# Performance work log

Hardware: AMD Instinct MI355X
Metric: run time of the kernel (lower is better)

Reference implementation:

```python
import jax, jax.numpy as jnp
import numpy as np

N = 4096
E = 131072
IN_CH, E_CH, HID, OUT = 512, 64, 256, 16
K, J = 2, 3
REWEIGHT = ((E_CH + HID) / (IN_CH + HID)) ** 0.5


def gcn(x, W, b, src, dst, dinv):
    # x: [B, N, F] -> [B, N, H]; symmetric-normalized aggregation with self-loops (PyG GCNConv)
    h = x @ W
    norm = dinv[src] * dinv[dst]                      # [E]
    msg = jnp.take(h, src, axis=-2) * norm[:, None]   # [B, E, H]
    agg = jnp.zeros_like(h).at[:, dst, :].add(msg)
    out = agg + h * (dinv * dinv)[:, None]            # self-loop term, norm_ii = deg_i^-1
    return out + b


def setup_inputs() -> dict:
    key = jax.random.key(0)
    ks = jax.random.split(key, 12)
    x = jax.random.normal(ks[0], (1, N, IN_CH), jnp.float32)
    edge_index = jax.random.randint(ks[1], (2, E), 0, N)
    e_noise = jax.random.normal(ks[2], (K + J, N, E_CH), jnp.float32)
    eps = jax.random.normal(ks[3], (J, N, OUT), jnp.float32)
    def glorot(k, fan_in, fan_out):
        s = (6.0 / (fan_in + fan_out)) ** 0.5
        return jax.random.uniform(k, (fan_in, fan_out), jnp.float32, -s, s)
    W1 = glorot(ks[4], IN_CH, HID); b1 = jnp.zeros((HID,), jnp.float32)
    We = glorot(ks[5], E_CH, HID); be = jnp.zeros((HID,), jnp.float32)
    Wmu = glorot(ks[6], HID, OUT); bmu = jnp.zeros((OUT,), jnp.float32)
    Wsig = glorot(ks[7], HID, OUT); bsig = jnp.zeros((OUT,), jnp.float32)
    rk_lgt = jax.random.uniform(ks[8], (1, OUT), jnp.float32, -6.0, 0.0)
    return {"x": x, "edge_index": edge_index, "e_noise": e_noise, "eps": eps,
            "W1": W1, "b1": b1, "We": We, "be": be,
            "Wmu": Wmu, "bmu": bmu, "Wsig": Wsig, "bsig": bsig, "rk_lgt": rk_lgt}


def reference(x, edge_index, e_noise, eps, W1, b1, We, be, Wmu, bmu, Wsig, bsig, rk_lgt):
    src, dst = edge_index[0], edge_index[1]
    deg = jnp.zeros((N,), jnp.float32).at[dst].add(1.0) + 1.0  # self-loops
    dinv = jax.lax.rsqrt(deg)

    hidden_x = jax.nn.relu(gcn(x, W1, b1, src, dst, dinv))          # [1, N, HID]
    e = e_noise * REWEIGHT                                          # [K+J, N, E_CH]
    hidden_e = gcn(e, We, be, src, dst, dinv)                       # [K+J, N, HID]
    hidden1 = hidden_x + hidden_e                                   # [K+J, N, HID]

    p_signal = jnp.mean(hidden_x ** 2)
    p_noise = jnp.mean(hidden_e ** 2, axis=(-2, -1))                # [K+J]
    snr = p_signal / p_noise

    mu = gcn(hidden1, Wmu, bmu, src, dst, dinv)                     # [K+J, N, OUT]
    sigma = gcn(hidden1, Wsig, bsig, src, dst, dinv)                # [K+J, N, OUT]

    emb_mu = mu[K:]
    emb_logvar = sigma[K:]
    std = jnp.exp(emb_logvar * 0.5)
    z = eps * std + emb_mu                                          # [J, N, OUT]

    # GraphDecoder, gdc='ip', dropout=0 (eval): z_scaled = z, adj = sigmoid(z z^T)
    rk = jnp.sqrt(jax.nn.sigmoid(rk_lgt))                           # [1, OUT]
    adj_lgt = jnp.einsum('bnd,bmd->bnm', z, z)                      # [J, N, N]
    adj_ = jax.nn.sigmoid(adj_lgt)
    z_scaled = z
    return (adj_, mu, sigma, z, z_scaled, eps, rk, snr)
```

## Files before the change

### kernel.cpp

```cpp
#include <hip/hip_runtime.h>

#define NN     4096
#define NE     131072
#define IN_CH  512
#define E_CH   64
#define HID    256
#define OUT_CH 16
#define KK     2
#define JJ     3
#define NB     5
#define REWEIGHT 0.6454972243679028f

#define O_ADJ  0L
#define O_MU   50331648L
#define O_SG   50659328L
#define O_Z    50987008L
#define O_ZS   51183616L
#define O_EPS  51380224L
#define O_RK   51576832L
#define O_SNR  51576848L


__global__ void k_deg(const int* __restrict__ dst, int* __restrict__ degi) {
    int i = blockIdx.x * 256 + threadIdx.x;
    if (i < NE) atomicAdd(&degi[dst[i]], 1);
}

__global__ void k_scan(const int* __restrict__ degi, int* __restrict__ rowptr,
                       int* __restrict__ cursor) {
    __shared__ int sums[1024];
    int t = threadIdx.x;
    int v[4];
    int s = 0;
#pragma unroll
    for (int i = 0; i < 4; ++i) { v[i] = s; s += degi[t * 4 + i]; }
    sums[t] = s;
    __syncthreads();
    for (int off = 1; off < 1024; off <<= 1) {
        int a = (t >= off) ? sums[t - off] : 0;
        __syncthreads();
        sums[t] += a;
        __syncthreads();
    }
    int base = (t > 0) ? sums[t - 1] : 0;
#pragma unroll
    for (int i = 0; i < 4; ++i) {
        rowptr[t * 4 + i] = base + v[i];
        cursor[t * 4 + i] = base + v[i];
    }
    if (t == 1023) rowptr[4096] = sums[1023];
}

__global__ void k_dinv(const int* __restrict__ degi, float* __restrict__ dinv) {
    int i = blockIdx.x * 256 + threadIdx.x;
    if (i < NN) dinv[i] = rsqrtf((float)degi[i] + 1.0f);
}

__global__ void k_fill(const int* __restrict__ src, const int* __restrict__ dst,
                       const float* __restrict__ dinv,
                       int* __restrict__ cursor, int* __restrict__ esrc,
                       float* __restrict__ enorm) {
    int i = blockIdx.x * 256 + threadIdx.x;
    if (i >= NE) return;
    int s = src[i], d = dst[i];
    int pos = atomicAdd(&cursor[d], 1);
    esrc[pos] = s;
    enorm[pos] = dinv[s] * dinv[d];
}


__global__ void k_gemm_x(const float* __restrict__ x, const float* __restrict__ W1,
                         float* __restrict__ h) {
    __shared__ float xs[4][IN_CH];
    long r0 = (long)blockIdx.x * 4;
    int c = threadIdx.x;
    for (int idx = c; idx < 4 * IN_CH; idx += 256) {
        int rr = idx >> 9, k = idx & 511;
        xs[rr][k] = x[(r0 + rr) * IN_CH + k];
    }
    __syncthreads();
    float acc[4] = {};
#pragma unroll 4
    for (int k = 0; k < IN_CH; ++k) {
        float w = W1[k * HID + c];
#pragma unroll
        for (int rr = 0; rr < 4; ++rr) acc[rr] = fmaf(xs[rr][k], w, acc[rr]);
    }
#pragma unroll
    for (int rr = 0; rr < 4; ++rr) h[(r0 + rr) * HID + c] = acc[rr];
}

__global__ void __launch_bounds__(64) k_agg_e(const float* __restrict__ e,
                        const int* __restrict__ rowptr, const int* __restrict__ esrc,
                        const float* __restrict__ enorm, const float* __restrict__ dinv,
                        float* __restrict__ u) {
    int n = blockIdx.x, b = blockIdx.y;
    int c = threadIdx.x;
    int beg = rowptr[n], end = rowptr[n + 1];
    float dv = dinv[n];
    const float* eb = &e[(long)b * NN * E_CH];
    float acc = eb[(long)n * E_CH + c] * dv * dv;
    for (int j = beg; j < end; ++j)
        acc = fmaf(eb[(long)esrc[j] * E_CH + c], enorm[j], acc);
    u[((long)b * NN + n) * E_CH + c] = acc * REWEIGHT;
}

__global__ void k_gemm_e(const float* __restrict__ u, const float* __restrict__ We,
                         const float* __restrict__ be, float* __restrict__ he,
                         float* __restrict__ psum) {
    __shared__ float us[8][E_CH];
    long r0 = (long)blockIdx.x * 8;
    int c = threadIdx.x;
    for (int idx = c; idx < 8 * E_CH; idx += 256) {
        int rr = idx >> 6, k = idx & 63;
        us[rr][k] = u[(r0 + rr) * E_CH + k];
    }
    __syncthreads();
    float acc[8] = {};
#pragma unroll
    for (int k = 0; k < E_CH; ++k) {
        float w = We[k * HID + c];
#pragma unroll
        for (int rr = 0; rr < 8; ++rr) acc[rr] = fmaf(us[rr][k], w, acc[rr]);
    }
    float bias = be[c];
    float sq = 0.f;
#pragma unroll
    for (int rr = 0; rr < 8; ++rr) {
        float v = acc[rr] + bias;
        he[(r0 + rr) * HID + c] = v;
        sq += v * v;
    }
#pragma unroll
    for (int off = 32; off; off >>= 1) sq += __shfl_down(sq, off, 64);
    __shared__ float red[4];
    if ((threadIdx.x & 63) == 0) red[threadIdx.x >> 6] = sq;
    __syncthreads();
    if (threadIdx.x == 0) {
        int b = blockIdx.x >> 9;
        atomicAdd(&psum[1 + b], red[0] + red[1] + red[2] + red[3]);
    }
}

__global__ void k_agg_x(const float* __restrict__ h, const int* __restrict__ rowptr,
                        const int* __restrict__ esrc, const float* __restrict__ enorm,
                        const float* __restrict__ dinv, const float* __restrict__ b1,
                        float* __restrict__ hx, float* __restrict__ psum) {
    int n = blockIdx.x;
    int c = threadIdx.x;
    int beg = rowptr[n], end = rowptr[n + 1];
    float dv = dinv[n];
    float acc = h[(long)n * HID + c] * dv * dv + b1[c];
    for (int j = beg; j < end; ++j)
        acc = fmaf(h[(long)esrc[j] * HID + c], enorm[j], acc);
    acc = fmaxf(acc, 0.f);
    hx[(long)n * HID + c] = acc;
    float sq = acc * acc;
#pragma unroll
    for (int off = 32; off; off >>= 1) sq += __shfl_down(sq, off, 64);
    __shared__ float red[4];
    if ((threadIdx.x & 63) == 0) red[threadIdx.x >> 6] = sq;
    __syncthreads();
    if (threadIdx.x == 0) atomicAdd(&psum[0], red[0] + red[1] + red[2] + red[3]);
}

__global__ void k_gemm_ms(const float* __restrict__ hx, const float* __restrict__ he,
                          const float* __restrict__ Wmu, const float* __restrict__ Wsg,
                          float* __restrict__ hmu, float* __restrict__ hsg) {
    int o = threadIdx.x & 15;
    int nn = threadIdx.x >> 4;
    int n = blockIdx.x * 16 + nn;
    int b = blockIdx.y;
    const float* px = &hx[(long)n * HID];
    const float* pe = &he[((long)b * NN + n) * HID];
    float amu = 0.f, asg = 0.f;
#pragma unroll 4
    for (int k = 0; k < HID; ++k) {
        float h1 = px[k] + pe[k];
        amu = fmaf(h1, Wmu[k * OUT_CH + o], amu);
        asg = fmaf(h1, Wsg[k * OUT_CH + o], asg);
    }
    long idx = ((long)b * NN + n) * OUT_CH + o;
    hmu[idx] = amu;
    hsg[idx] = asg;
}

__global__ void k_agg16(const int* __restrict__ rowptr, const int* __restrict__ esrc,
                        const float* __restrict__ enorm, const float* __restrict__ dinv,
                        const float* __restrict__ hmu, const float* __restrict__ hsg,
                        const float* __restrict__ bmu, const float* __restrict__ bsg,
                        float* __restrict__ omu, float* __restrict__ osg) {
    int n = blockIdx.x, b = blockIdx.y;
    int t = threadIdx.x;
    int es = t >> 4, c = t & 15;
    int beg = rowptr[n], end = rowptr[n + 1];
    const float* pm = &hmu[(long)b * NN * OUT_CH];
    const float* ps = &hsg[(long)b * NN * OUT_CH];
    float am = 0.f, as = 0.f;
    for (int j = beg + es; j < end; j += 16) {
        int s = esrc[j];
        float w = enorm[j];
        am = fmaf(pm[(long)s * OUT_CH + c], w, am);
        as = fmaf(ps[(long)s * OUT_CH + c], w, as);
    }
    am += __shfl_xor(am, 16, 64); as += __shfl_xor(as, 16, 64);
    am += __shfl_xor(am, 32, 64); as += __shfl_xor(as, 32, 64);
    __shared__ float rm[4][16], rs[4][16];
    int w = t >> 6;
    if ((t & 63) < 16) { rm[w][t & 15] = am; rs[w][t & 15] = as; }
    __syncthreads();
    float dv = dinv[n];
    float d2 = dv * dv;
    long base = ((long)b * NN + n) * OUT_CH;
    if (t < 16) {
        float v = rm[0][t] + rm[1][t] + rm[2][t] + rm[3][t]
                + pm[(long)n * OUT_CH + t] * d2 + bmu[t];
        omu[base + t] = v;
    } else if (t < 32) {
        int c2 = t - 16;
        float v = rs[0][c2] + rs[1][c2] + rs[2][c2] + rs[3][c2]
                + ps[(long)n * OUT_CH + c2] * d2 + bsg[c2];
        osg[base + c2] = v;
    }
}


__global__ void k_z(const float* __restrict__ omu, const float* __restrict__ osg,
                    const float* __restrict__ eps,
                    float* __restrict__ oz, float* __restrict__ ozs, float* __restrict__ oeps) {
    long i = (long)blockIdx.x * 256 + threadIdx.x;
    float mu = omu[(long)KK * NN * OUT_CH + i];
    float lv = osg[(long)KK * NN * OUT_CH + i];
    float ep = eps[i];
    float z = fmaf(ep, expf(0.5f * lv), mu);
    oz[i] = z;
    ozs[i] = z;
    oeps[i] = ep;
}

__global__ void k_tail(const float* __restrict__ rk_lgt, const float* __restrict__ psum,
                       float* __restrict__ ork, float* __restrict__ osnr) {
    int t = threadIdx.x;
    if (t < 16) ork[t] = sqrtf(1.f / (1.f + expf(-rk_lgt[t])));
    if (t >= 16 && t < 16 + NB) osnr[t - 16] = psum[0] / psum[1 + (t - 16)];
}

__global__ void k_adj(const float* __restrict__ z, float* __restrict__ adj) {
    __shared__ float za[64][17];
    __shared__ float zb[64][17];
    int b  = blockIdx.z;
    int bi = blockIdx.y;
    int bj = blockIdx.x;
    const float* zbase = &z[(long)b * NN * OUT_CH];
    int tid = threadIdx.x;
    for (int l = tid; l < 64 * 16; l += 256) {
        int r = l >> 4, c = l & 15;
        za[r][c] = zbase[((long)bi * 64 + r) * OUT_CH + c];
        zb[r][c] = zbase[((long)bj * 64 + r) * OUT_CH + c];
    }
    __syncthreads();
    int tr = tid >> 4, tc = tid & 15;
    float acc[4][4] = {};
#pragma unroll
    for (int d = 0; d < OUT_CH; ++d) {
        float av[4], bv[4];
#pragma unroll
        for (int i = 0; i < 4; ++i) av[i] = za[tr * 4 + i][d];
#pragma unroll
        for (int j = 0; j < 4; ++j) bv[j] = zb[tc * 4 + j][d];
#pragma unroll
        for (int i = 0; i < 4; ++i)
#pragma unroll
            for (int j = 0; j < 4; ++j) acc[i][j] = fmaf(av[i], bv[j], acc[i][j]);
    }
#pragma unroll
    for (int i = 0; i < 4; ++i) {
        long row = (long)bi * 64 + tr * 4 + i;
        float4 o;
        o.x = 1.f / (1.f + expf(-acc[i][0]));
        o.y = 1.f / (1.f + expf(-acc[i][1]));
        o.z = 1.f / (1.f + expf(-acc[i][2]));
        o.w = 1.f / (1.f + expf(-acc[i][3]));
        *reinterpret_cast<float4*>(&adj[((long)b * NN + row) * NN + (long)bj * 64 + tc * 4]) = o;
    }
}


extern "C" void kernel_launch(void* const* d_in, const int* in_sizes, int n_in,
                              void* d_out, int out_size, void* d_ws, size_t ws_size,
                              hipStream_t stream) {
    const float* x      = (const float*)d_in[0];
    const int*   eidx   = (const int*)d_in[1];
    const float* enoise = (const float*)d_in[2];
    const float* eps    = (const float*)d_in[3];
    const float* W1     = (const float*)d_in[4];
    const float* b1     = (const float*)d_in[5];
    const float* We     = (const float*)d_in[6];
    const float* be     = (const float*)d_in[7];
    const float* Wmu    = (const float*)d_in[8];
    const float* bmu    = (const float*)d_in[9];
    const float* Wsg    = (const float*)d_in[10];
    const float* bsg    = (const float*)d_in[11];
    const float* rk_lgt = (const float*)d_in[12];

    const int* src = eidx;
    const int* dst = eidx + NE;

    float* out = (float*)d_out;
    char*  ws  = (char*)d_ws;

    int*   degi   = (int*)ws;
    int*   rowptr = degi + 4096;
    int*   cursor = rowptr + 4097 + 3;
    int*   esrc   = cursor + 4096;
    float* enorm  = (float*)(esrc + NE);
    float* dinv   = enorm + NE;
    float* psum   = dinv + 4096;
    float* h_x    = psum + 16;
    float* hx     = h_x + (long)NN * HID;
    float* u_e    = hx + (long)NN * HID;
    float* he     = u_e + (long)NB * NN * E_CH;
    float* h_mu   = he + (long)NB * NN * HID;
    float* h_sg   = h_mu + (long)NB * NN * OUT_CH;

    float* omu = out + O_MU;
    float* osg = out + O_SG;

    hipMemsetAsync(degi, 0, NN * sizeof(int), stream);
    hipMemsetAsync(psum, 0, 16 * sizeof(float), stream);

    k_deg<<<NE / 256, 256, 0, stream>>>(dst, degi);
    k_scan<<<1, 1024, 0, stream>>>(degi, rowptr, cursor);
    k_dinv<<<NN / 256, 256, 0, stream>>>(degi, dinv);
    k_fill<<<NE / 256, 256, 0, stream>>>(src, dst, dinv, cursor, esrc, enorm);

    k_gemm_x<<<NN / 4, 256, 0, stream>>>(x, W1, h_x);
    k_agg_x<<<NN, 256, 0, stream>>>(h_x, rowptr, esrc, enorm, dinv, b1, hx, psum);

    k_agg_e<<<dim3(NN, NB), 64, 0, stream>>>(enoise, rowptr, esrc, enorm, dinv, u_e);
    k_gemm_e<<<NB * NN / 8, 256, 0, stream>>>(u_e, We, be, he, psum);

    k_gemm_ms<<<dim3(NN / 16, NB), 256, 0, stream>>>(hx, he, Wmu, Wsg, h_mu, h_sg);
    k_agg16<<<dim3(NN, NB), 256, 0, stream>>>(rowptr, esrc, enorm, dinv,
                                              h_mu, h_sg, bmu, bsg, omu, osg);

    k_z<<<(long)JJ * NN * OUT_CH / 256, 256, 0, stream>>>(omu, osg, eps,
                                                          out + O_Z, out + O_ZS, out + O_EPS);
    k_tail<<<1, 64, 0, stream>>>(rk_lgt, psum, out + O_RK, out + O_SNR);

    k_adj<<<dim3(NN / 64, NN / 64, JJ), 256, 0, stream>>>(out + O_Z, out);
}
```

Baseline: 549.9 us.

## Fuse small kernels, batch edge aggregation, enlarge adjacency tiles with fast sigmoid

Folds dinv computation into the scan kernel and the rk/snr tail into k_z, removing two launches. k_agg_e now handles all five noise batches per node so the edge indices and weights are read once. k_agg16 gives each node a single wavefront, which drops the shared-memory reduction and the barrier. k_adj moves to 128x128 tiles with transposed shared memory and 8x8 register blocking, and replaces expf plus division with __expf and a hardware reciprocal. k_gemm_x processes 8 rows per block. The fast sigmoid is slightly less accurate, and the larger register tiles raise register pressure.

```diff
diff --git a/kernel.cpp b/kernel.cpp
--- a/kernel.cpp
+++ b/kernel.cpp
@@ -20,20 +20,26 @@
 #define O_RK   51576832L
 #define O_SNR  51576848L
 
+__device__ __forceinline__ float fast_sigmoid(float x) {
+    float e = __expf(-x);
+    return __builtin_amdgcn_rcpf(1.f + e);
+}
+
 
 __global__ void k_deg(const int* __restrict__ dst, int* __restrict__ degi) {
     int i = blockIdx.x * 256 + threadIdx.x;
     if (i < NE) atomicAdd(&degi[dst[i]], 1);
 }
 
-__global__ void k_scan(const int* __restrict__ degi, int* __restrict__ rowptr,
-                       int* __restrict__ cursor) {
+__global__ void __launch_bounds__(1024) k_scan(const int* __restrict__ degi,
+                       int* __restrict__ rowptr, int* __restrict__ cursor,
+                       float* __restrict__ dinv) {
     __shared__ int sums[1024];
     int t = threadIdx.x;
-    int v[4];
+    int d0[4], v[4];
     int s = 0;
 #pragma unroll
-    for (int i = 0; i < 4; ++i) { v[i] = s; s += degi[t * 4 + i]; }
+    for (int i = 0; i < 4; ++i) { d0[i] = degi[t * 4 + i]; v[i] = s; s += d0[i]; }
     sums[t] = s;
     __syncthreads();
     for (int off = 1; off < 1024; off <<= 1) {
@@ -47,13 +53,9 @@
     for (int i = 0; i < 4; ++i) {
         rowptr[t * 4 + i] = base + v[i];
         cursor[t * 4 + i] = base + v[i];
+        dinv[t * 4 + i] = rsqrtf((float)d0[i] + 1.0f);
     }
     if (t == 1023) rowptr[4096] = sums[1023];
-}
-
-__global__ void k_dinv(const int* __restrict__ degi, float* __restrict__ dinv) {
-    int i = blockIdx.x * 256 + threadIdx.x;
-    if (i < NN) dinv[i] = rsqrtf((float)degi[i] + 1.0f);
 }
 
 __global__ void k_fill(const int* __restrict__ src, const int* __restrict__ dst,
@@ -69,80 +71,29 @@
 }
 
 
-__global__ void k_gemm_x(const float* __restrict__ x, const float* __restrict__ W1,
-                         float* __restrict__ h) {
-    __shared__ float xs[4][IN_CH];
-    long r0 = (long)blockIdx.x * 4;
+__global__ void __launch_bounds__(256) k_gemm_x(const float* __restrict__ x,
+                         const float* __restrict__ W1, float* __restrict__ h) {
+    __shared__ float xs[8][IN_CH];
+    long r0 = (long)blockIdx.x * 8;
     int c = threadIdx.x;
-    for (int idx = c; idx < 4 * IN_CH; idx += 256) {
+    for (int idx = c; idx < 8 * IN_CH; idx += 256) {
         int rr = idx >> 9, k = idx & 511;
         xs[rr][k] = x[(r0 + rr) * IN_CH + k];
     }
     __syncthreads();
-    float acc[4] = {};
+    float acc[8] = {};
 #pragma unroll 4
     for (int k = 0; k < IN_CH; ++k) {
         float w = W1[k * HID + c];
 #pragma unroll
-        for (int rr = 0; rr < 4; ++rr) acc[rr] = fmaf(xs[rr][k], w, acc[rr]);
-    }
-#pragma unroll
-    for (int rr = 0; rr < 4; ++rr) h[(r0 + rr) * HID + c] = acc[rr];
-}
-
-__global__ void __launch_bounds__(64) k_agg_e(const float* __restrict__ e,
-                        const int* __restrict__ rowptr, const int* __restrict__ esrc,
-                        const float* __restrict__ enorm, const float* __restrict__ dinv,
-                        float* __restrict__ u) {
-    int n = blockIdx.x, b = blockIdx.y;
-    int c = threadIdx.x;
-    int beg = rowptr[n], end = rowptr[n + 1];
-    float dv = dinv[n];
-    const float* eb = &e[(long)b * NN * E_CH];
-    float acc = eb[(long)n * E_CH + c] * dv * dv;
-    for (int j = beg; j < end; ++j)
-        acc = fmaf(eb[(long)esrc[j] * E_CH + c], enorm[j], acc);
-    u[((long)b * NN + n) * E_CH + c] = acc * REWEIGHT;
-}
-
-__global__ void k_gemm_e(const float* __restrict__ u, const float* __restrict__ We,
-                         const float* __restrict__ be, float* __restrict__ he,
-                         float* __restrict__ psum) {
-    __shared__ float us[8][E_CH];
-    long r0 = (long)blockIdx.x * 8;
-    int c = threadIdx.x;
-    for (int idx = c; idx < 8 * E_CH; idx += 256) {
-        int rr = idx >> 6, k = idx & 63;
-        us[rr][k] = u[(r0 + rr) * E_CH + k];
-    }
-    __syncthreads();
-    float acc[8] = {};
-#pragma unroll
-    for (int k = 0; k < E_CH; ++k) {
-        float w = We[k * HID + c];
-#pragma unroll
-        for (int rr = 0; rr < 8; ++rr) acc[rr] = fmaf(us[rr][k], w, acc[rr]);
-    }
-    float bias = be[c];
-    float sq = 0.f;
-#pragma unroll
-    for (int rr = 0; rr < 8; ++rr) {
-        float v = acc[rr] + bias;
-        he[(r0 + rr) * HID + c] = v;
-        sq += v * v;
-    }
-#pragma unroll
-    for (int off = 32; off; off >>= 1) sq += __shfl_down(sq, off, 64);
-    __shared__ float red[4];
-    if ((threadIdx.x & 63) == 0) red[threadIdx.x >> 6] = sq;
-    __syncthreads();
-    if (threadIdx.x == 0) {
-        int b = blockIdx.x >> 9;
-        atomicAdd(&psum[1 + b], red[0] + red[1] + red[2] + red[3]);
-    }
-}
-
-__global__ void k_agg_x(const float* __restrict__ h, const int* __restrict__ rowptr,
+        for (int rr = 0; rr < 8; ++rr) acc[rr] = fmaf(xs[rr][k], w, acc[rr]);
+    }
+#pragma unroll
+    for (int rr = 0; rr < 8; ++rr) h[(r0 + rr) * HID + c] = acc[rr];
+}
+
+__global__ void __launch_bounds__(256) k_agg_x(const float* __restrict__ h,
+                        const int* __restrict__ rowptr,
                         const int* __restrict__ esrc, const float* __restrict__ enorm,
                         const float* __restrict__ dinv, const float* __restrict__ b1,
                         float* __restrict__ hx, float* __restrict__ psum) {
@@ -164,7 +115,70 @@
     if (threadIdx.x == 0) atomicAdd(&psum[0], red[0] + red[1] + red[2] + red[3]);
 }
 
-__global__ void k_gemm_ms(const float* __restrict__ hx, const float* __restrict__ he,
+__global__ void __launch_bounds__(256) k_agg_e(const float* __restrict__ e,
+                        const int* __restrict__ rowptr, const int* __restrict__ esrc,
+                        const float* __restrict__ enorm, const float* __restrict__ dinv,
+                        float* __restrict__ u) {
+    int n = blockIdx.x * 4 + (threadIdx.x >> 6);
+    int c = threadIdx.x & 63;
+    int beg = rowptr[n], end = rowptr[n + 1];
+    float dv = dinv[n];
+    float d2 = dv * dv;
+    float acc[NB];
+#pragma unroll
+    for (int b = 0; b < NB; ++b) acc[b] = e[((long)b * NN + n) * E_CH + c] * d2;
+    for (int j = beg; j < end; ++j) {
+        int s = esrc[j];
+        float w = enorm[j];
+        long base = (long)s * E_CH + c;
+#pragma unroll
+        for (int b = 0; b < NB; ++b)
+            acc[b] = fmaf(e[(long)b * NN * E_CH + base], w, acc[b]);
+    }
+#pragma unroll
+    for (int b = 0; b < NB; ++b) u[((long)b * NN + n) * E_CH + c] = acc[b] * REWEIGHT;
+}
+
+__global__ void __launch_bounds__(256) k_gemm_e(const float* __restrict__ u,
+                         const float* __restrict__ We,
+                         const float* __restrict__ be, float* __restrict__ he,
+                         float* __restrict__ psum) {
+    __shared__ float us[8][E_CH];
+    long r0 = (long)blockIdx.x * 8;
+    int c = threadIdx.x;
+    for (int idx = c; idx < 8 * E_CH; idx += 256) {
+        int rr = idx >> 6, k = idx & 63;
+        us[rr][k] = u[(r0 + rr) * E_CH + k];
+    }
+    __syncthreads();
+    float acc[8] = {};
+#pragma unroll
+    for (int k = 0; k < E_CH; ++k) {
+        float w = We[k * HID + c];
+#pragma unroll
+        for (int rr = 0; rr < 8; ++rr) acc[rr] = fmaf(us[rr][k], w, acc[rr]);
+    }
+    float bias = be[c];
+    float sq = 0.f;
+#pragma unroll
+    for (int rr = 0; rr < 8; ++rr) {
+        float v = acc[rr] + bias;
+        he[(r0 + rr) * HID + c] = v;
+        sq += v * v;
+    }
+#pragma unroll
+    for (int off = 32; off; off >>= 1) sq += __shfl_down(sq, off, 64);
+    __shared__ float red[4];
+    if ((threadIdx.x & 63) == 0) red[threadIdx.x >> 6] = sq;
+    __syncthreads();
+    if (threadIdx.x == 0) {
+        int b = blockIdx.x >> 9;
+        atomicAdd(&psum[1 + b], red[0] + red[1] + red[2] + red[3]);
+    }
+}
+
+__global__ void __launch_bounds__(256) k_gemm_ms(const float* __restrict__ hx,
+                          const float* __restrict__ he,
                           const float* __restrict__ Wmu, const float* __restrict__ Wsg,
                           float* __restrict__ hmu, float* __restrict__ hsg) {
     int o = threadIdx.x & 15;
@@ -185,19 +199,22 @@
     hsg[idx] = asg;
 }
 
-__global__ void k_agg16(const int* __restrict__ rowptr, const int* __restrict__ esrc,
+__global__ void __launch_bounds__(256) k_agg16(const int* __restrict__ rowptr,
+                        const int* __restrict__ esrc,
                         const float* __restrict__ enorm, const float* __restrict__ dinv,
                         const float* __restrict__ hmu, const float* __restrict__ hsg,
                         const float* __restrict__ bmu, const float* __restrict__ bsg,
                         float* __restrict__ omu, float* __restrict__ osg) {
-    int n = blockIdx.x, b = blockIdx.y;
-    int t = threadIdx.x;
-    int es = t >> 4, c = t & 15;
+    int p = blockIdx.x * 4 + (threadIdx.x >> 6);
+    int lane = threadIdx.x & 63;
+    int n = p & (NN - 1);
+    int b = p >> 12;
+    int es = lane >> 4, c = lane & 15;
     int beg = rowptr[n], end = rowptr[n + 1];
     const float* pm = &hmu[(long)b * NN * OUT_CH];
     const float* ps = &hsg[(long)b * NN * OUT_CH];
     float am = 0.f, as = 0.f;
-    for (int j = beg + es; j < end; j += 16) {
+    for (int j = beg + es; j < end; j += 4) {
         int s = esrc[j];
         float w = enorm[j];
         am = fmaf(pm[(long)s * OUT_CH + c], w, am);
@@ -205,29 +222,22 @@
     }
     am += __shfl_xor(am, 16, 64); as += __shfl_xor(as, 16, 64);
     am += __shfl_xor(am, 32, 64); as += __shfl_xor(as, 32, 64);
-    __shared__ float rm[4][16], rs[4][16];
-    int w = t >> 6;
-    if ((t & 63) < 16) { rm[w][t & 15] = am; rs[w][t & 15] = as; }
-    __syncthreads();
     float dv = dinv[n];
     float d2 = dv * dv;
     long base = ((long)b * NN + n) * OUT_CH;
-    if (t < 16) {
-        float v = rm[0][t] + rm[1][t] + rm[2][t] + rm[3][t]
-                + pm[(long)n * OUT_CH + t] * d2 + bmu[t];
-        omu[base + t] = v;
-    } else if (t < 32) {
-        int c2 = t - 16;
-        float v = rs[0][c2] + rs[1][c2] + rs[2][c2] + rs[3][c2]
-                + ps[(long)n * OUT_CH + c2] * d2 + bsg[c2];
-        osg[base + c2] = v;
+    if (lane < 16) {
+        omu[base + c] = am + pm[(long)n * OUT_CH + c] * d2 + bmu[c];
+    } else if (lane < 32) {
+        osg[base + c] = as + ps[(long)n * OUT_CH + c] * d2 + bsg[c];
     }
 }
 
 
 __global__ void k_z(const float* __restrict__ omu, const float* __restrict__ osg,
                     const float* __restrict__ eps,
-                    float* __restrict__ oz, float* __restrict__ ozs, float* __restrict__ oeps) {
+                    float* __restrict__ oz, float* __restrict__ ozs, float* __restrict__ oeps,
+                    const float* __restrict__ rk_lgt, const float* __restrict__ psum,
+                    float* __restrict__ ork, float* __restrict__ osnr) {
     long i = (long)blockIdx.x * 256 + threadIdx.x;
     float mu = omu[(long)KK * NN * OUT_CH + i];
     float lv = osg[(long)KK * NN * OUT_CH + i];
@@ -236,52 +246,54 @@
     oz[i] = z;
     ozs[i] = z;
     oeps[i] = ep;
-}
-
-__global__ void k_tail(const float* __restrict__ rk_lgt, const float* __restrict__ psum,
-                       float* __restrict__ ork, float* __restrict__ osnr) {
-    int t = threadIdx.x;
-    if (t < 16) ork[t] = sqrtf(1.f / (1.f + expf(-rk_lgt[t])));
-    if (t >= 16 && t < 16 + NB) osnr[t - 16] = psum[0] / psum[1 + (t - 16)];
-}
-
-__global__ void k_adj(const float* __restrict__ z, float* __restrict__ adj) {
-    __shared__ float za[64][17];
-    __shared__ float zb[64][17];
+    if (blockIdx.x == 0) {
+        int t = threadIdx.x;
+        if (t < 16) ork[t] = sqrtf(1.f / (1.f + expf(-rk_lgt[t])));
+        if (t >= 16 && t < 16 + NB) osnr[t - 16] = psum[0] / psum[1 + (t - 16)];
+    }
+}
+
+__global__ void __launch_bounds__(256) k_adj(const float* __restrict__ z,
+                                             float* __restrict__ adj) {
+    __shared__ float zaT[16][132];
+    __shared__ float zbT[16][132];
     int b  = blockIdx.z;
     int bi = blockIdx.y;
     int bj = blockIdx.x;
     const float* zbase = &z[(long)b * NN * OUT_CH];
     int tid = threadIdx.x;
-    for (int l = tid; l < 64 * 16; l += 256) {
+    for (int l = tid; l < 128 * 16; l += 256) {
         int r = l >> 4, c = l & 15;
-        za[r][c] = zbase[((long)bi * 64 + r) * OUT_CH + c];
-        zb[r][c] = zbase[((long)bj * 64 + r) * OUT_CH + c];
+        zaT[c][r] = zbase[((long)bi * 128 + r) * OUT_CH + c];
+        zbT[c][r] = zbase[((long)bj * 128 + r) * OUT_CH + c];
     }
     __syncthreads();
     int tr = tid >> 4, tc = tid & 15;
-    float acc[4][4] = {};
+    float acc[8][8] = {};
 #pragma unroll
     for (int d = 0; d < OUT_CH; ++d) {
-        float av[4], bv[4];
-#pragma unroll
-        for (int i = 0; i < 4; ++i) av[i] = za[tr * 4 + i][d];
-#pragma unroll
-        for (int j = 0; j < 4; ++j) bv[j] = zb[tc * 4 + j][d];
-#pragma unroll
-        for (int i = 0; i < 4; ++i)
-#pragma unroll
-            for (int j = 0; j < 4; ++j) acc[i][j] = fmaf(av[i], bv[j], acc[i][j]);
-    }
-#pragma unroll
-    for (int i = 0; i < 4; ++i) {
-        long row = (long)bi * 64 + tr * 4 + i;
-        float4 o;
-        o.x = 1.f / (1.f + expf(-acc[i][0]));
-        o.y = 1.f / (1.f + expf(-acc[i][1]));
-        o.z = 1.f / (1.f + expf(-acc[i][2]));
-        o.w = 1.f / (1.f + expf(-acc[i][3]));
-        *reinterpret_cast<float4*>(&adj[((long)b * NN + row) * NN + (long)bj * 64 + tc * 4]) = o;
+        float4 a0 = *reinterpret_cast<const float4*>(&zaT[d][tr * 8]);
+        float4 a1 = *reinterpret_cast<const float4*>(&zaT[d][tr * 8 + 4]);
+        float4 b0 = *reinterpret_cast<const float4*>(&zbT[d][tc * 8]);
+        float4 b1 = *reinterpret_cast<const float4*>(&zbT[d][tc * 8 + 4]);
+        float av[8] = {a0.x, a0.y, a0.z, a0.w, a1.x, a1.y, a1.z, a1.w};
+        float bv[8] = {b0.x, b0.y, b0.z, b0.w, b1.x, b1.y, b1.z, b1.w};
+#pragma unroll
+        for (int i = 0; i < 8; ++i)
+#pragma unroll
+            for (int j = 0; j < 8; ++j) acc[i][j] = fmaf(av[i], bv[j], acc[i][j]);
+    }
+#pragma unroll
+    for (int i = 0; i < 8; ++i) {
+        long row = (long)bi * 128 + tr * 8 + i;
+        float* orow = &adj[((long)b * NN + row) * NN + (long)bj * 128 + tc * 8];
+        float4 o0, o1;
+        o0.x = fast_sigmoid(acc[i][0]); o0.y = fast_sigmoid(acc[i][1]);
+        o0.z = fast_sigmoid(acc[i][2]); o0.w = fast_sigmoid(acc[i][3]);
+        o1.x = fast_sigmoid(acc[i][4]); o1.y = fast_sigmoid(acc[i][5]);
+        o1.z = fast_sigmoid(acc[i][6]); o1.w = fast_sigmoid(acc[i][7]);
+        *reinterpret_cast<float4*>(&orow[0]) = o0;
+        *reinterpret_cast<float4*>(&orow[4]) = o1;
     }
 }
 
@@ -330,23 +342,22 @@
     hipMemsetAsync(psum, 0, 16 * sizeof(float), stream);
 
     k_deg<<<NE / 256, 256, 0, stream>>>(dst, degi);
-    k_scan<<<1, 1024, 0, stream>>>(degi, rowptr, cursor);
-    k_dinv<<<NN / 256, 256, 0, stream>>>(degi, dinv);
+    k_scan<<<1, 1024, 0, stream>>>(degi, rowptr, cursor, dinv);
     k_fill<<<NE / 256, 256, 0, stream>>>(src, dst, dinv, cursor, esrc, enorm);
 
-    k_gemm_x<<<NN / 4, 256, 0, stream>>>(x, W1, h_x);
+    k_gemm_x<<<NN / 8, 256, 0, stream>>>(x, W1, h_x);
     k_agg_x<<<NN, 256, 0, stream>>>(h_x, rowptr, esrc, enorm, dinv, b1, hx, psum);
 
-    k_agg_e<<<dim3(NN, NB), 64, 0, stream>>>(enoise, rowptr, esrc, enorm, dinv, u_e);
+    k_agg_e<<<NN / 4, 256, 0, stream>>>(enoise, rowptr, esrc, enorm, dinv, u_e);
     k_gemm_e<<<NB * NN / 8, 256, 0, stream>>>(u_e, We, be, he, psum);
 
     k_gemm_ms<<<dim3(NN / 16, NB), 256, 0, stream>>>(hx, he, Wmu, Wsg, h_mu, h_sg);
-    k_agg16<<<dim3(NN, NB), 256, 0, stream>>>(rowptr, esrc, enorm, dinv,
-                                              h_mu, h_sg, bmu, bsg, omu, osg);
+    k_agg16<<<NB * NN / 4, 256, 0, stream>>>(rowptr, esrc, enorm, dinv,
+                                             h_mu, h_sg, bmu, bsg, omu, osg);
 
     k_z<<<(long)JJ * NN * OUT_CH / 256, 256, 0, stream>>>(omu, osg, eps,
-                                                          out + O_Z, out + O_ZS, out + O_EPS);
-    k_tail<<<1, 64, 0, stream>>>(rk_lgt, psum, out + O_RK, out + O_SNR);
-
-    k_adj<<<dim3(NN / 64, NN / 64, JJ), 256, 0, stream>>>(out + O_Z, out);
-}
+                                                          out + O_Z, out + O_ZS, out + O_EPS,
+                                                          rk_lgt, psum, out + O_RK, out + O_SNR);
+
+    k_adj<<<dim3(NN / 128, NN / 128, JJ), 256, 0, stream>>>(out + O_Z, out);
+}
```

After: 543.3 us. About the same (-1.2%).
